# Kernel tuning notes

Measured on AMD Instinct MI355X. Metric: run time of the kernel, lower is better.

The kernel has to match this reference:

```python
import jax, jax.numpy as jnp
import numpy as np

D_MODEL, N_HEAD, D_HEAD = 1024, 16, 64
B, QLEN, MLEN = 4, 1024, 1024
KLEN = QLEN + MLEN  # == rlen
NEG_INF = -1e30


def _rel_shift(x):
    # x: [b, q, rlen, n] -> Transformer-XL relative shift along axis 2
    b, q, rl, n = x.shape
    zero_pad = jnp.zeros((b, q, 1, n), dtype=x.dtype)
    x_padded = jnp.concatenate([zero_pad, x], axis=2)          # [b, q, rl+1, n]
    x_padded = x_padded.reshape(b, rl + 1, q, n)
    return x_padded[:, 1:].reshape(b, q, rl, n)


def setup_inputs() -> dict:
    key = jax.random.key(0)
    ks = jax.random.split(key, 8)
    s = 1.0 / np.sqrt(D_MODEL)
    w = jax.random.normal(ks[0], (B, KLEN, D_MODEL), jnp.float32)
    r = jax.random.normal(ks[1], (1, KLEN, D_MODEL), jnp.float32)
    Wq = jax.random.normal(ks[2], (D_MODEL, N_HEAD * D_HEAD), jnp.float32) * s
    Wkv = jax.random.normal(ks[3], (D_MODEL, 2 * N_HEAD * D_HEAD), jnp.float32) * s
    Wr = jax.random.normal(ks[4], (D_MODEL, N_HEAD * D_HEAD), jnp.float32) * s
    Wo = jax.random.normal(ks[5], (N_HEAD * D_HEAD, D_MODEL), jnp.float32) * s
    bias_w = jax.random.normal(ks[6], (N_HEAD, D_HEAD), jnp.float32) * 0.02
    bias_r = jax.random.normal(ks[7], (N_HEAD, D_HEAD), jnp.float32) * 0.02
    # causal-with-memory mask: query i attends to keys j <= i + MLEN
    i = jnp.arange(QLEN)[:, None]
    j = jnp.arange(KLEN)[None, :]
    attn_mask = j > (i + MLEN)  # True => masked
    return {"w": w, "r": r, "Wq": Wq, "Wkv": Wkv, "Wr": Wr, "Wo": Wo,
            "bias_w": bias_w, "bias_r": bias_r, "attn_mask": attn_mask,
            "qlen": QLEN}


def reference(w, r, Wq, Wkv, Wr, Wo, bias_w, bias_r, attn_mask, qlen):
    bsz, klen, _ = w.shape
    rlen = r.shape[1]
    scale = 1.0 / np.sqrt(D_HEAD)

    q = (w[:, -qlen:] @ Wq).reshape(bsz, qlen, N_HEAD, D_HEAD)
    kv = w @ Wkv
    k, v = jnp.split(kv, 2, axis=-1)
    k = k.reshape(bsz, klen, N_HEAD, D_HEAD)
    v = v.reshape(bsz, klen, N_HEAD, D_HEAD)
    rk = (r @ Wr).reshape(rlen, N_HEAD, D_HEAD)

    AC = jnp.einsum('bind,bjnd->bijn', q + bias_w, k)
    BD = jnp.einsum('bind,jnd->bijn', q + bias_r, rk)
    score = (AC + _rel_shift(BD)) * scale
    score = jnp.where(attn_mask[None, :, :, None], NEG_INF, score)
    prob = jax.nn.softmax(score, axis=2)
    attn_vec = jnp.einsum('bijn,bjnd->bind', prob, v)
    attn_vec = attn_vec.reshape(bsz, qlen, N_HEAD * D_HEAD)
    return attn_vec @ Wo
```

## Files before the change

### kernel.cpp

```cpp
#include <hip/hip_runtime.h>
#include <hip/hip_bf16.h>
#include <stdint.h>


#define DEVI static __device__ __forceinline__

typedef __attribute__((ext_vector_type(8))) short  s8v;
typedef __attribute__((ext_vector_type(4))) float  f4v;
typedef __attribute__((ext_vector_type(2))) int    i2v;
typedef __attribute__((ext_vector_type(4))) float  fl4;

DEVI unsigned short f2b(float f) {
  __hip_bfloat16 h = __float2bfloat16(f);
  return __builtin_bit_cast(unsigned short, h);
}

DEVI f4v MFMA(s8v a, s8v b, f4v c) {
  return __builtin_amdgcn_mfma_f32_16x16x32_bf16(a, b, c, 0, 0, 0);
}

DEVI void gl_lds16(const void* g, void* lds) {
  __builtin_amdgcn_global_load_lds(
      (const __attribute__((address_space(1))) unsigned int*)g,
      (__attribute__((address_space(3))) unsigned int*)lds, 16, 0, 0);
}

__global__ void transpose_all(const float* __restrict__ Wq,
                              const float* __restrict__ Wkv,
                              const float* __restrict__ Wr,
                              const float* __restrict__ Wo,
                              unsigned short* __restrict__ WqT,
                              unsigned short* __restrict__ WkvT,
                              unsigned short* __restrict__ WrT,
                              unsigned short* __restrict__ WoT) {
  __shared__ float tile[32][33];
  const int bx = blockIdx.x;
  const float* W;
  unsigned short* WT;
  int N, nb;
  if (bx < 32)       { W = Wq;  WT = WqT;  N = 1024; nb = bx; }
  else if (bx < 96)  { W = Wkv; WT = WkvT; N = 2048; nb = bx - 32; }
  else if (bx < 128) { W = Wr;  WT = WrT;  N = 1024; nb = bx - 96; }
  else               { W = Wo;  WT = WoT;  N = 1024; nb = bx - 128; }
  int n0 = nb * 32, k0 = blockIdx.y * 32;
  int tx = threadIdx.x, ty = threadIdx.y;
#pragma unroll
  for (int i = 0; i < 4; ++i)
    tile[ty + i * 8][tx] = W[(size_t)(k0 + ty + i * 8) * N + n0 + tx];
  __syncthreads();
#pragma unroll
  for (int i = 0; i < 4; ++i)
    WT[(size_t)(n0 + ty + i * 8) * 1024 + k0 + tx] = f2b(tile[tx][ty + i * 8]);
}

__global__ void transpose_v(const unsigned short* __restrict__ in,
                            unsigned short* __restrict__ out) {
  __shared__ unsigned short Ts[64 * 72];
  const int t = threadIdx.x;
  const int j0 = blockIdx.x * 64;
  const size_t bh = blockIdx.y;
#pragma unroll
  for (int p = 0; p < 2; ++p) {
    int cc = t + p * 256;
    int j = cc >> 3, d0 = (cc & 7) * 8;
    s8v v = *(const s8v*)(in + (bh * 2048 + j0 + j) * 64 + d0);
    *(s8v*)(Ts + j * 72 + d0) = v;
  }
  __syncthreads();
  const int d = t >> 2, jc = (t & 3) * 16;
  s8v a, b;
#pragma unroll
  for (int e = 0; e < 8; ++e) a[e] = (short)Ts[(jc + e) * 72 + d];
#pragma unroll
  for (int e = 0; e < 8; ++e) b[e] = (short)Ts[(jc + 8 + e) * 72 + d];
  *(s8v*)(out + (bh * 64 + d) * 2048 + j0 + jc) = a;
  *(s8v*)(out + (bh * 64 + d) * 2048 + j0 + jc + 8) = b;
}

template <int MODE>
__global__ __launch_bounds__(256, 2) void gemm_kern(
    const float* __restrict__ A, const unsigned short* __restrict__ A16,
    const unsigned short* __restrict__ BT, unsigned short* __restrict__ O1,
    unsigned short* __restrict__ O2, float* __restrict__ Of,
    const float* __restrict__ biasw, const float* __restrict__ biasr) {
  __shared__ unsigned short As[2][128 * 32];
  __shared__ unsigned short Bs[2][128 * 32];
  const int t = threadIdx.x, l = t & 63, w = t >> 6;
  const int g = l >> 4, lr = l & 15;
  const int bm = blockIdx.x, bn = blockIdx.y;
  const int wr = w >> 1, wc = w & 1;
  f4v acc[4][4] = {};

  auto stageB = [&](int k0, int buf) {
#pragma unroll
    for (int ss = 0; ss < 2; ++ss) {
      int idx = w * 64 + ss * 256 + l;
      int row = idx >> 2, c = idx & 3;
      gl_lds16(BT + (size_t)(bn * 128 + row) * 1024 + k0 + c * 8,
               (void*)(Bs[buf] + (w * 64 + ss * 256) * 8));
    }
  };
  auto stageA_lds = [&](int k0, int buf) {
#pragma unroll
    for (int ss = 0; ss < 2; ++ss) {
      int idx = w * 64 + ss * 256 + l;
      int row = idx >> 2, c = idx & 3;
      gl_lds16(A16 + (size_t)(bm * 128 + row) * 1024 + k0 + c * 8,
               (void*)(As[buf] + (w * 64 + ss * 256) * 8));
    }
  };
  auto loadA = [&](int k0, fl4* regs) {
#pragma unroll
    for (int ss = 0; ss < 4; ++ss) {
      int idx = t + ss * 256;
      int row = idx >> 3, c = idx & 7;
      int grow = bm * 128 + row;
      size_t arow = (MODE == 0)
                        ? ((size_t)(grow >> 10) * 2048 + 1024 + (grow & 1023))
                        : (size_t)grow;
      regs[ss] = *(const fl4*)(A + arow * 1024 + k0 + c * 4);
    }
  };
  auto writeA = [&](const fl4* regs, int buf) {
#pragma unroll
    for (int ss = 0; ss < 4; ++ss) {
      int idx = t + ss * 256;
      int row = idx >> 3, c = idx & 7;
      fl4 v = regs[ss];
      unsigned int p0 = f2b(v.x) | ((unsigned int)f2b(v.y) << 16);
      unsigned int p1 = f2b(v.z) | ((unsigned int)f2b(v.w) << 16);
      i2v pv; pv.x = (int)p0; pv.y = (int)p1;
      *(i2v*)(As[buf] + row * 32 + c * 4) = pv;
    }
  };

  stageB(0, 0);
  if (MODE == 3) {
    stageA_lds(0, 0);
  } else {
    fl4 r0[4];
    loadA(0, r0);
    writeA(r0, 0);
  }
  __syncthreads();

  int cur = 0;
  for (int step = 0; step < 32; ++step) {
    const bool nx = step < 31;
    const int nk0 = (step + 1) * 32;
    fl4 aregs[4];
    if (nx) {
      stageB(nk0, cur ^ 1);
      if (MODE == 3) stageA_lds(nk0, cur ^ 1);
      else loadA(nk0, aregs);
    }
    s8v af[4], bf[4];
#pragma unroll
    for (int m = 0; m < 4; ++m)
      af[m] = *(const s8v*)(As[cur] + (wr * 64 + m * 16 + lr) * 32 + g * 8);
#pragma unroll
    for (int n = 0; n < 4; ++n)
      bf[n] = *(const s8v*)(Bs[cur] + (wc * 64 + n * 16 + lr) * 32 + g * 8);
#pragma unroll
    for (int m = 0; m < 4; ++m)
#pragma unroll
      for (int n = 0; n < 4; ++n) acc[m][n] = MFMA(af[m], bf[n], acc[m][n]);
    if (nx && MODE != 3) writeA(aregs, cur ^ 1);
    __syncthreads();
    cur ^= 1;
  }

#pragma unroll
  for (int m = 0; m < 4; ++m) {
#pragma unroll
    for (int n = 0; n < 4; ++n) {
#pragma unroll
      for (int r = 0; r < 4; ++r) {
        int row = bm * 128 + wr * 64 + m * 16 + g * 4 + r;
        int col = bn * 128 + wc * 64 + n * 16 + lr;
        float v = acc[m][n][r];
        if (MODE == 0) {
          int b = row >> 10, i = row & 1023;
          int nh = col >> 6, d = col & 63;
          size_t o = ((size_t)(b * 16 + nh) * 1024 + i) * 64 + d;
          O1[o] = f2b(v + biasw[col]);
          O2[o] = f2b(v + biasr[col]);
        } else if (MODE == 1) {
          int b = row >> 11, j = row & 2047;
          if (col < 1024)
            O1[((size_t)(b * 16 + (col >> 6)) * 2048 + j) * 64 + (col & 63)] =
                f2b(v);
          else
            O2[((size_t)(b * 16 + ((col - 1024) >> 6)) * 2048 + j) * 64 +
               (col & 63)] = f2b(v);
        } else if (MODE == 2) {
          O1[((size_t)(col >> 6) * 2048 + row) * 64 + (col & 63)] = f2b(v);
        } else {
          Of[(size_t)row * 1024 + col] = v;
        }
      }
    }
  }
}

__global__ __launch_bounds__(256, 2) void attn_kern(
    const unsigned short* __restrict__ qw, const unsigned short* __restrict__ qr,
    const unsigned short* __restrict__ kk, const unsigned short* __restrict__ vt,
    const unsigned short* __restrict__ rkp, unsigned short* __restrict__ av) {
  __shared__ unsigned short Ks[2][64 * 64];
  __shared__ unsigned short Vs[2][64 * 64];
  __shared__ unsigned short Rs[2][128 * 64];
  __shared__ unsigned short Pn[4][1024];
  const int t = threadIdx.x, l = t & 63, w = t >> 6;
  const int g = l >> 4, lr = l & 15;
  const int i0 = blockIdx.x * 64, n = blockIdx.y, b = blockIdx.z;
  const size_t bn = (size_t)(b * 16 + n);
  const unsigned short* qwb = qw + bn * 1024 * 64;
  const unsigned short* qrb = qr + bn * 1024 * 64;
  const unsigned short* kb = kk + bn * 2048 * 64;
  const unsigned short* vb = vt + bn * 64 * 2048;
  const unsigned short* rb = rkp + (size_t)n * 2048 * 64;

  const int qi = i0 + w * 16 + lr;
  s8v aqw[2], aqr[2];
#pragma unroll
  for (int ks = 0; ks < 2; ++ks) {
    aqw[ks] = *(const s8v*)(qwb + (size_t)qi * 64 + ks * 32 + g * 8);
    aqr[ks] = *(const s8v*)(qrb + (size_t)qi * 64 + ks * 32 + g * 8);
  }

  f4v acco[4] = {};
  float mrow[4] = {-3e38f, -3e38f, -3e38f, -3e38f};
  float lrow[4] = {};

  const float SC = 0.18033688f;
  const int ntile = (i0 + 1088) >> 6;

  auto stage = [&](int jt, int buf) {
    const int j0 = jt * 64;
    const int m0 = j0 + 960 - i0;
#pragma unroll
    for (int ss = 0; ss < 2; ++ss) {
      int idx = w * 64 + ss * 256 + l;
      int row = idx >> 3, c = idx & 7;
      gl_lds16(kb + (size_t)(j0 + row) * 64 + ((c ^ (row & 7)) * 8),
               (void*)(Ks[buf] + (w * 64 + ss * 256) * 8));
    }
#pragma unroll
    for (int ss = 0; ss < 2; ++ss) {
      int idx = w * 64 + ss * 256 + l;
      int d = idx >> 3, c = idx & 7;
      gl_lds16(vb + (size_t)d * 2048 + j0 + ((c ^ (d & 7)) * 8),
               (void*)(Vs[buf] + (w * 64 + ss * 256) * 8));
    }
#pragma unroll
    for (int ss = 0; ss < 4; ++ss) {
      int idx = w * 64 + ss * 256 + l;
      int rr = idx >> 3, c = idx & 7;
      int m = m0 + rr;
      if (m > 2047) m = 2047;
      gl_lds16(rb + (size_t)m * 64 + ((c ^ (rr & 7)) * 8),
               (void*)(Rs[buf] + (w * 64 + ss * 256) * 8));
    }
  };

  stage(0, 0);
  __syncthreads();

  int cur = 0;
  for (int jt = 0; jt < ntile; ++jt) {
    const int j0 = jt * 64;
    if (jt + 1 < ntile) stage(jt + 1, cur ^ 1);
    const bool mt = (jt == ntile - 1);

    f4v accs[4] = {};
    f4v acce[5] = {};
#pragma unroll
    for (int ks = 0; ks < 2; ++ks) {
#pragma unroll
      for (int jf = 0; jf < 4; ++jf) {
        int row = jf * 16 + lr;
        s8v bk =
            *(const s8v*)(Ks[cur] + row * 64 + (((ks * 4 + g) ^ (row & 7)) * 8));
        accs[jf] = MFMA(aqw[ks], bk, accs[jf]);
      }
#pragma unroll
      for (int ef = 0; ef < 5; ++ef) {
        int row = (3 - w + ef) * 16 + lr;
        s8v br =
            *(const s8v*)(Rs[cur] + row * 64 + (((ks * 4 + g) ^ (row & 7)) * 8));
        acce[ef] = MFMA(aqr[ks], br, acce[ef]);
      }
    }

    float P[4][4];
    float corr[4];
#pragma unroll
    for (int r = 0; r < 4; ++r) {
      const int s = 15 - 4 * g - r;
      const int src = (l & 48) | ((lr + s) & 15);
      const int carry = (lr + s) >> 4;
      float rmax = -3e38f;
#pragma unroll
      for (int jf = 0; jf < 4; ++jf) {
        float e0 = __shfl(acce[jf][r], src, 64);
        float e1 = __shfl(acce[jf + 1][r], src, 64);
        float ev = carry ? e1 : e0;
        float sv = (accs[jf][r] + ev) * SC;
        if (mt) {
          int jg = j0 + jf * 16 + lr;
          int ig = i0 + w * 16 + 4 * g + r;
          if (jg > ig + 1024) sv = -3e38f;
        }
        P[jf][r] = sv;
        rmax = fmaxf(rmax, sv);
      }
#pragma unroll
      for (int dd = 1; dd < 16; dd <<= 1)
        rmax = fmaxf(rmax, __shfl_xor(rmax, dd, 64));
      float nm = fmaxf(mrow[r], rmax);
      corr[r] = exp2f(mrow[r] - nm);
      mrow[r] = nm;
      float psum = 0.f;
#pragma unroll
      for (int jf = 0; jf < 4; ++jf) {
        float p = exp2f(P[jf][r] - nm);
        P[jf][r] = p;
        psum += p;
      }
#pragma unroll
      for (int dd = 1; dd < 16; dd <<= 1) psum += __shfl_xor(psum, dd, 64);
      lrow[r] = lrow[r] * corr[r] + psum;
    }
#pragma unroll
    for (int df = 0; df < 4; ++df)
#pragma unroll
      for (int r = 0; r < 4; ++r) acco[df][r] *= corr[r];

#pragma unroll
    for (int jf = 0; jf < 4; ++jf) {
#pragma unroll
      for (int r = 0; r < 4; ++r) {
        int ip = 4 * g + r;
        int cj = (jf * 2 + (lr >> 3)) ^ (ip & 7);
        Pn[w][ip * 64 + cj * 8 + (lr & 7)] = f2b(P[jf][r]);
      }
    }
    asm volatile("s_waitcnt lgkmcnt(0)" ::: "memory");
    __builtin_amdgcn_sched_barrier(0);

#pragma unroll
    for (int ks = 0; ks < 2; ++ks) {
      s8v ap =
          *(const s8v*)(Pn[w] + lr * 64 + (((ks * 4 + g) ^ (lr & 7)) * 8));
#pragma unroll
      for (int df = 0; df < 4; ++df) {
        int vrow = df * 16 + lr;
        s8v bv = *(const s8v*)(Vs[cur] + vrow * 64 +
                               (((ks * 4 + g) ^ (vrow & 7)) * 8));
        acco[df] = MFMA(ap, bv, acco[df]);
      }
    }
    __syncthreads();
    cur ^= 1;
  }

#pragma unroll
  for (int r = 0; r < 4; ++r) {
    float inv = 1.0f / lrow[r];
    int ig = i0 + w * 16 + 4 * g + r;
#pragma unroll
    for (int df = 0; df < 4; ++df)
      av[((size_t)b * 1024 + ig) * 1024 + n * 64 + df * 16 + lr] =
          f2b(acco[df][r] * inv);
  }
}

extern "C" void kernel_launch(void* const* d_in, const int* in_sizes, int n_in,
                              void* d_out, int out_size, void* d_ws,
                              size_t ws_size, hipStream_t stream) {
  (void)in_sizes; (void)n_in; (void)out_size; (void)ws_size;
  const float* w   = (const float*)d_in[0];
  const float* r   = (const float*)d_in[1];
  const float* Wq  = (const float*)d_in[2];
  const float* Wkv = (const float*)d_in[3];
  const float* Wr  = (const float*)d_in[4];
  const float* Wo  = (const float*)d_in[5];
  const float* bw  = (const float*)d_in[6];
  const float* br  = (const float*)d_in[7];

  char* ws = (char*)d_ws;
  const size_t MB = 1024 * 1024;
  unsigned short* WqT  = (unsigned short*)(ws + 0 * MB);
  unsigned short* WkvT = (unsigned short*)(ws + 2 * MB);
  unsigned short* WrT  = (unsigned short*)(ws + 6 * MB);
  unsigned short* WoT  = (unsigned short*)(ws + 8 * MB);
  unsigned short* qwb  = (unsigned short*)(ws + 10 * MB);
  unsigned short* qrb  = (unsigned short*)(ws + 18 * MB);
  unsigned short* kbf  = (unsigned short*)(ws + 26 * MB);
  unsigned short* vbf  = (unsigned short*)(ws + 42 * MB);
  unsigned short* rkb  = (unsigned short*)(ws + 58 * MB);
  unsigned short* avb  = (unsigned short*)(ws + 62 * MB);
  unsigned short* vtb  = (unsigned short*)d_out;

  hipLaunchKernelGGL(transpose_all, dim3(160, 32), dim3(32, 8), 0, stream,
                     Wq, Wkv, Wr, Wo, WqT, WkvT, WrT, WoT);

  hipLaunchKernelGGL((gemm_kern<0>), dim3(32, 8), dim3(256), 0, stream,
                     w, (const unsigned short*)nullptr, WqT, qwb, qrb,
                     (float*)nullptr, bw, br);
  hipLaunchKernelGGL((gemm_kern<1>), dim3(64, 16), dim3(256), 0, stream,
                     w, (const unsigned short*)nullptr, WkvT, kbf, vbf,
                     (float*)nullptr, (const float*)nullptr,
                     (const float*)nullptr);
  hipLaunchKernelGGL((gemm_kern<2>), dim3(16, 8), dim3(256), 0, stream,
                     r, (const unsigned short*)nullptr, WrT, rkb,
                     (unsigned short*)nullptr, (float*)nullptr,
                     (const float*)nullptr, (const float*)nullptr);

  hipLaunchKernelGGL(transpose_v, dim3(32, 64), dim3(256), 0, stream, vbf, vtb);

  hipLaunchKernelGGL(attn_kern, dim3(16, 16, 4), dim3(256), 0, stream,
                     qwb, qrb, kbf, vtb, rkb, avb);

  hipLaunchKernelGGL((gemm_kern<3>), dim3(32, 8), dim3(256), 0, stream,
                     (const float*)nullptr, avb, WoT, (unsigned short*)nullptr,
                     (unsigned short*)nullptr, (float*)d_out,
                     (const float*)nullptr, (const float*)nullptr);
}
```

Measured before the change: 469.9 us.

## Single-buffer attention LDS for higher occupancy, lazy softmax rescale, MFMA row sums

Folds the softmax scale into the Q projection epilogue so the attention kernel no longer multiplies by the scale. Replaces double-buffered K/V/R tiles with single buffers and raises launch bounds to 4 blocks per CU, relying on occupancy instead of in-block prefetch to hide latency. Softmax rescaling is skipped unless the tile max exceeds the running max by more than a threshold, and the row sum is computed with an MFMA against a ones vector instead of shuffle reductions. Query tiles are permuted across blocks to balance the causal work. Losing the prefetch exposes load latency within each block, and the lazy rescale allows exponent growth up to 2^8.

```diff
diff --git a/kernel.cpp b/kernel.cpp
--- a/kernel.cpp
+++ b/kernel.cpp
@@ -89,6 +89,7 @@
   const int g = l >> 4, lr = l & 15;
   const int bm = blockIdx.x, bn = blockIdx.y;
   const int wr = w >> 1, wc = w & 1;
+  const float QSC = 0.18033688f;
   f4v acc[4][4] = {};
 
   auto stageB = [&](int k0, int buf) {
@@ -183,8 +184,8 @@
           int b = row >> 10, i = row & 1023;
           int nh = col >> 6, d = col & 63;
           size_t o = ((size_t)(b * 16 + nh) * 1024 + i) * 64 + d;
-          O1[o] = f2b(v + biasw[col]);
-          O2[o] = f2b(v + biasr[col]);
+          O1[o] = f2b((v + biasw[col]) * QSC);
+          O2[o] = f2b((v + biasr[col]) * QSC);
         } else if (MODE == 1) {
           int b = row >> 11, j = row & 2047;
           if (col < 1024)
@@ -203,17 +204,18 @@
   }
 }
 
-__global__ __launch_bounds__(256, 2) void attn_kern(
+__global__ __launch_bounds__(256, 4) void attn_kern(
     const unsigned short* __restrict__ qw, const unsigned short* __restrict__ qr,
     const unsigned short* __restrict__ kk, const unsigned short* __restrict__ vt,
     const unsigned short* __restrict__ rkp, unsigned short* __restrict__ av) {
-  __shared__ unsigned short Ks[2][64 * 64];
-  __shared__ unsigned short Vs[2][64 * 64];
-  __shared__ unsigned short Rs[2][128 * 64];
+  __shared__ unsigned short Ks[64 * 64];
+  __shared__ unsigned short Vs[64 * 64];
+  __shared__ unsigned short Rs[128 * 64];
   __shared__ unsigned short Pn[4][1024];
   const int t = threadIdx.x, l = t & 63, w = t >> 6;
   const int g = l >> 4, lr = l & 15;
-  const int i0 = blockIdx.x * 64, n = blockIdx.y, b = blockIdx.z;
+  const int i0 = ((blockIdx.x * 5) & 15) * 64;
+  const int n = blockIdx.y, b = blockIdx.z;
   const size_t bn = (size_t)(b * 16 + n);
   const unsigned short* qwb = qw + bn * 1024 * 64;
   const unsigned short* qrb = qr + bn * 1024 * 64;
@@ -229,14 +231,17 @@
     aqr[ks] = *(const s8v*)(qrb + (size_t)qi * 64 + ks * 32 + g * 8);
   }
 
+  s8v ONES;
+#pragma unroll
+  for (int e = 0; e < 8; ++e) ONES[e] = (short)0x3F80;
+
   f4v acco[4] = {};
+  f4v accl = {};
   float mrow[4] = {-3e38f, -3e38f, -3e38f, -3e38f};
-  float lrow[4] = {};
-
-  const float SC = 0.18033688f;
+
   const int ntile = (i0 + 1088) >> 6;
 
-  auto stage = [&](int jt, int buf) {
+  auto stage = [&](int jt) {
     const int j0 = jt * 64;
     const int m0 = j0 + 960 - i0;
 #pragma unroll
@@ -244,14 +249,14 @@
       int idx = w * 64 + ss * 256 + l;
       int row = idx >> 3, c = idx & 7;
       gl_lds16(kb + (size_t)(j0 + row) * 64 + ((c ^ (row & 7)) * 8),
-               (void*)(Ks[buf] + (w * 64 + ss * 256) * 8));
+               (void*)(Ks + (w * 64 + ss * 256) * 8));
     }
 #pragma unroll
     for (int ss = 0; ss < 2; ++ss) {
       int idx = w * 64 + ss * 256 + l;
       int d = idx >> 3, c = idx & 7;
       gl_lds16(vb + (size_t)d * 2048 + j0 + ((c ^ (d & 7)) * 8),
-               (void*)(Vs[buf] + (w * 64 + ss * 256) * 8));
+               (void*)(Vs + (w * 64 + ss * 256) * 8));
     }
 #pragma unroll
     for (int ss = 0; ss < 4; ++ss) {
@@ -260,17 +265,14 @@
       int m = m0 + rr;
       if (m > 2047) m = 2047;
       gl_lds16(rb + (size_t)m * 64 + ((c ^ (rr & 7)) * 8),
-               (void*)(Rs[buf] + (w * 64 + ss * 256) * 8));
+               (void*)(Rs + (w * 64 + ss * 256) * 8));
     }
   };
 
-  stage(0, 0);
-  __syncthreads();
-
-  int cur = 0;
   for (int jt = 0; jt < ntile; ++jt) {
     const int j0 = jt * 64;
-    if (jt + 1 < ntile) stage(jt + 1, cur ^ 1);
+    stage(jt);
+    __syncthreads();
     const bool mt = (jt == ntile - 1);
 
     f4v accs[4] = {};
@@ -281,61 +283,54 @@
       for (int jf = 0; jf < 4; ++jf) {
         int row = jf * 16 + lr;
         s8v bk =
-            *(const s8v*)(Ks[cur] + row * 64 + (((ks * 4 + g) ^ (row & 7)) * 8));
+            *(const s8v*)(Ks + row * 64 + (((ks * 4 + g) ^ (row & 7)) * 8));
         accs[jf] = MFMA(aqw[ks], bk, accs[jf]);
       }
 #pragma unroll
       for (int ef = 0; ef < 5; ++ef) {
         int row = (3 - w + ef) * 16 + lr;
         s8v br =
-            *(const s8v*)(Rs[cur] + row * 64 + (((ks * 4 + g) ^ (row & 7)) * 8));
+            *(const s8v*)(Rs + row * 64 + (((ks * 4 + g) ^ (row & 7)) * 8));
         acce[ef] = MFMA(aqr[ks], br, acce[ef]);
       }
     }
 
     float P[4][4];
-    float corr[4];
 #pragma unroll
     for (int r = 0; r < 4; ++r) {
       const int s = 15 - 4 * g - r;
       const int src = (l & 48) | ((lr + s) & 15);
       const int carry = (lr + s) >> 4;
-      float rmax = -3e38f;
+      float es[5];
+#pragma unroll
+      for (int f = 0; f < 5; ++f) es[f] = __shfl(acce[f][r], src, 64);
+      float pmax = -3e38f;
 #pragma unroll
       for (int jf = 0; jf < 4; ++jf) {
-        float e0 = __shfl(acce[jf][r], src, 64);
-        float e1 = __shfl(acce[jf + 1][r], src, 64);
-        float ev = carry ? e1 : e0;
-        float sv = (accs[jf][r] + ev) * SC;
+        float sv = accs[jf][r] + (carry ? es[jf + 1] : es[jf]);
         if (mt) {
           int jg = j0 + jf * 16 + lr;
           int ig = i0 + w * 16 + 4 * g + r;
           if (jg > ig + 1024) sv = -3e38f;
         }
         P[jf][r] = sv;
-        rmax = fmaxf(rmax, sv);
-      }
-#pragma unroll
-      for (int dd = 1; dd < 16; dd <<= 1)
-        rmax = fmaxf(rmax, __shfl_xor(rmax, dd, 64));
-      float nm = fmaxf(mrow[r], rmax);
-      corr[r] = exp2f(mrow[r] - nm);
-      mrow[r] = nm;
-      float psum = 0.f;
-#pragma unroll
-      for (int jf = 0; jf < 4; ++jf) {
-        float p = exp2f(P[jf][r] - nm);
-        P[jf][r] = p;
-        psum += p;
-      }
-#pragma unroll
-      for (int dd = 1; dd < 16; dd <<= 1) psum += __shfl_xor(psum, dd, 64);
-      lrow[r] = lrow[r] * corr[r] + psum;
-    }
-#pragma unroll
-    for (int df = 0; df < 4; ++df)
-#pragma unroll
-      for (int r = 0; r < 4; ++r) acco[df][r] *= corr[r];
+        pmax = fmaxf(pmax, sv);
+      }
+      if (!__all(pmax <= mrow[r] + 8.0f)) {
+        float rmax = pmax;
+#pragma unroll
+        for (int dd = 1; dd < 16; dd <<= 1)
+          rmax = fmaxf(rmax, __shfl_xor(rmax, dd, 64));
+        float nm = fmaxf(mrow[r], rmax);
+        float corr = exp2f(mrow[r] - nm);
+        mrow[r] = nm;
+#pragma unroll
+        for (int df = 0; df < 4; ++df) acco[df][r] *= corr;
+        accl[r] *= corr;
+      }
+#pragma unroll
+      for (int jf = 0; jf < 4; ++jf) P[jf][r] = exp2f(P[jf][r] - mrow[r]);
+    }
 
 #pragma unroll
     for (int jf = 0; jf < 4; ++jf) {
@@ -353,21 +348,21 @@
     for (int ks = 0; ks < 2; ++ks) {
       s8v ap =
           *(const s8v*)(Pn[w] + lr * 64 + (((ks * 4 + g) ^ (lr & 7)) * 8));
+      accl = MFMA(ap, ONES, accl);
 #pragma unroll
       for (int df = 0; df < 4; ++df) {
         int vrow = df * 16 + lr;
-        s8v bv = *(const s8v*)(Vs[cur] + vrow * 64 +
+        s8v bv = *(const s8v*)(Vs + vrow * 64 +
                                (((ks * 4 + g) ^ (vrow & 7)) * 8));
         acco[df] = MFMA(ap, bv, acco[df]);
       }
     }
     __syncthreads();
-    cur ^= 1;
   }
 
 #pragma unroll
   for (int r = 0; r < 4; ++r) {
-    float inv = 1.0f / lrow[r];
+    float inv = 1.0f / accl[r];
     int ig = i0 + w * 16 + 4 * g + r;
 #pragma unroll
     for (int df = 0; df < 4; ++df)
```

Result: slower. 758.3 us (+61.4%).
